# Performance work log

Hardware: AMD Instinct MI355X
Metric: run time of the kernel (lower is better)

## Reference

```python
import jax, jax.numpy as jnp
import numpy as np

B, S, H, D = 2, 2048, 16, 64
BS = 128          # block_size
NB = S // BS      # number of diagonal blocks
G = 128           # num_global_tokens
R = 64            # num_random_tokens
SCALE = 1.0 / float(D) ** 0.5


def setup_inputs() -> dict:
    key = jax.random.key(0)
    kq, kk, kv, kr = jax.random.split(key, 4)
    q = jax.random.normal(kq, (B, S, H, D), dtype=jnp.float32)
    k = jax.random.normal(kk, (B, S, H, D), dtype=jnp.float32)
    v = jax.random.normal(kv, (B, S, H, D), dtype=jnp.float32)
    attn_mask = jnp.zeros((B, H, S, S), dtype=jnp.float32)
    rand_indices = jax.random.randint(kr, (R,), 0, S, dtype=jnp.int32)
    return {"q": q, "k": k, "v": v, "attn_mask": attn_mask, "rand_indices": rand_indices}


def reference(q, k, v, attn_mask, rand_indices):
    # ---- diagonal block attention ----
    qb = q.reshape(B, NB, BS, H, D)
    kb = k.reshape(B, NB, BS, H, D)
    vb = v.reshape(B, NB, BS, H, D)
    scores = jnp.einsum('bnqhd,bnkhd->bnhqk', qb, kb) * SCALE  # (B,NB,H,BS,BS)
    mb = attn_mask.reshape(B, H, NB, BS, NB, BS)
    idx = jnp.arange(NB)
    diag = mb[:, :, idx, :, idx, :]                # (NB,B,H,BS,BS)
    scores = scores + jnp.transpose(diag, (1, 0, 2, 3, 4))
    w = jax.nn.softmax(scores, axis=-1)
    out = jnp.einsum('bnhqk,bnkhd->bnqhd', w, vb).reshape(B, S, H, D)

    # ---- global tokens attend to everything ----
    gq = q[:, :G]
    gv = v[:, :G]
    gs = jnp.einsum('bghd,bshd->bhgs', gq, k) * SCALE + attn_mask[:, :, :G, :]
    gw = jax.nn.softmax(gs, axis=-1)
    # faithful to torch einsum 'bhnm,bnhd->bnhd': v is indexed by the QUERY
    # axis, so this equals global_v * row-sum of softmax (== 1 numerically)
    out = out.at[:, :G].add(jnp.einsum('bhgs,bghd->bghd', gw, gv))

    # ---- random tokens attend to everything ----
    rq = q[:, rand_indices]                        # (B,R,H,D)
    rv = v[:, rand_indices]
    rs = jnp.einsum('brhd,bshd->bhrs', rq, k) * SCALE + attn_mask[:, :, rand_indices, :]
    rw = jax.nn.softmax(rs, axis=-1)
    # faithful to torch's size-1 broadcast in 'bhnm,bmhd->bnhd':
    # contribution = rand_v * row-sum of softmax
    rowsum = jnp.transpose(jnp.sum(rw, axis=-1), (0, 2, 1))  # (B,R,H)
    out = out.at[:, rand_indices].add(rv * rowsum[..., None])  # duplicate idx add, like the torch loop
    return out
```

## Files before the change

### kernel.cpp

```cpp
#include <hip/hip_runtime.h>
#include <stdint.h>

#define B_ 2
#define S_ 2048
#define H_ 16
#define D_ 64
#define BS_ 128
#define NB_ 16
#define R_ 64

typedef __bf16 bf16x8 __attribute__((ext_vector_type(8)));
typedef float f32x4 __attribute__((ext_vector_type(4)));

__device__ __forceinline__ uint16_t f2bf(float f) {
    uint32_t u = __builtin_bit_cast(uint32_t, f);
    u += 0x7fffu + ((u >> 16) & 1u);
    return (uint16_t)(u >> 16);
}

__global__ __launch_bounds__(256, 2) void bb_diag(
    const float* __restrict__ q, const float* __restrict__ k,
    const float* __restrict__ v, const float* __restrict__ mask,
    float* __restrict__ out)
{
    __shared__ __align__(16) uint8_t smem[49152];
    uint8_t* const k_lds  = smem;
    uint8_t* const p_lds  = smem;
    uint8_t* const vt_lds = smem + 32768;

    const int tid  = (int)threadIdx.x;
    const int w    = tid >> 6;
    const int lane = tid & 63;
    const int g    = lane >> 4;
    const int c    = lane & 15;

    const int blk = (int)blockIdx.x;
    const int h = blk & 15;
    const int n = (blk >> 4) & 15;
    const int b = blk >> 8;

    const int RS = H_ * D_;
    const size_t base = ((size_t)((b * S_ + n * BS_) * H_ + h)) * D_;
    const float* __restrict__ qg = q + base;
    const float* __restrict__ kg = k + base;
    const float* __restrict__ vg = v + base;
    float* __restrict__ og = out + base;

    #pragma unroll
    for (int it = 0; it < 8; ++it) {
        int i = it * 256 + tid;
        int row = i >> 4;
        int c4  = i & 15;
        f32x4 kv = *(const f32x4*)(kg + (size_t)row * RS + c4 * 4);
        uint32_t lo = (uint32_t)f2bf(kv[0]) | ((uint32_t)f2bf(kv[1]) << 16);
        uint32_t hi = (uint32_t)f2bf(kv[2]) | ((uint32_t)f2bf(kv[3]) << 16);
        uint32_t ka = ((uint32_t)(row * 128 + c4 * 8)) ^ ((row & 7) << 4);
        uint2 pk; pk.x = lo; pk.y = hi;
        *(uint2*)(k_lds + ka) = pk;

        f32x4 vv = *(const f32x4*)(vg + (size_t)row * RS + c4 * 4);
        #pragma unroll
        for (int jj = 0; jj < 4; ++jj) {
            int j = (jj + c4) & 3;
            int d = c4 * 4 + j;
            uint32_t va = ((uint32_t)(d * 256 + row * 2)) ^ ((d & 7) << 4);
            float vf = (j == 0) ? vv[0] : (j == 1) ? vv[1] : (j == 2) ? vv[2] : vv[3];
            *(uint16_t*)(vt_lds + va) = f2bf(vf);
        }
    }
    __syncthreads();

    bf16x8 qf[2][2];
    #pragma unroll
    for (int mt = 0; mt < 2; ++mt) {
        int row = (2 * w + mt) * 16 + c;
        const float* qrow = qg + (size_t)row * RS;
        #pragma unroll
        for (int ks = 0; ks < 2; ++ks) {
            const float* p0 = qrow + ks * 32 + g * 8;
            f32x4 x0 = *(const f32x4*)p0;
            f32x4 x1 = *(const f32x4*)(p0 + 4);
            union { bf16x8 v8; uint16_t us[8]; } cv;
            cv.us[0] = f2bf(x0[0]); cv.us[1] = f2bf(x0[1]);
            cv.us[2] = f2bf(x0[2]); cv.us[3] = f2bf(x0[3]);
            cv.us[4] = f2bf(x1[0]); cv.us[5] = f2bf(x1[1]);
            cv.us[6] = f2bf(x1[2]); cv.us[7] = f2bf(x1[3]);
            qf[mt][ks] = cv.v8;
        }
    }

    f32x4 acc[2][8];
    #pragma unroll
    for (int mt = 0; mt < 2; ++mt)
        #pragma unroll
        for (int nt = 0; nt < 8; ++nt)
            acc[mt][nt] = f32x4{0.f, 0.f, 0.f, 0.f};

    #pragma unroll
    for (int ks = 0; ks < 2; ++ks) {
        #pragma unroll
        for (int nt = 0; nt < 8; ++nt) {
            int krow = nt * 16 + c;
            uint32_t ka = ((uint32_t)(krow * 128 + ks * 64 + g * 16)) ^ ((krow & 7) << 4);
            bf16x8 bfr = *(const bf16x8*)(k_lds + ka);
            acc[0][nt] = __builtin_amdgcn_mfma_f32_16x16x32_bf16(qf[0][ks], bfr, acc[0][nt], 0, 0, 0);
            acc[1][nt] = __builtin_amdgcn_mfma_f32_16x16x32_bf16(qf[1][ks], bfr, acc[1][nt], 0, 0, 0);
        }
    }
    __syncthreads();

    const float* mb = mask + ((size_t)(b * H_ + h) * S_ + n * BS_) * S_ + (size_t)(n * BS_);
    float rcp_s[2][4];
    #pragma unroll
    for (int mt = 0; mt < 2; ++mt) {
        #pragma unroll
        for (int j = 0; j < 4; ++j) {
            int row = (2 * w + mt) * 16 + g * 4 + j;
            const float* mrow = mb + (size_t)row * S_;
            float s[8];
            float mx = -1e30f;
            #pragma unroll
            for (int nt = 0; nt < 8; ++nt) {
                s[nt] = acc[mt][nt][j] * 0.125f + mrow[nt * 16 + c];
                mx = fmaxf(mx, s[nt]);
            }
            #pragma unroll
            for (int t = 1; t < 16; t <<= 1) mx = fmaxf(mx, __shfl_xor(mx, t));
            float sum = 0.f;
            #pragma unroll
            for (int nt = 0; nt < 8; ++nt) {
                float p = __expf(s[nt] - mx);
                sum += p;
                uint32_t pa = ((uint32_t)(row * 256 + (nt * 16 + c) * 2)) ^ ((row & 7) << 4);
                *(uint16_t*)(p_lds + pa) = f2bf(p);
            }
            #pragma unroll
            for (int t = 1; t < 16; t <<= 1) sum += __shfl_xor(sum, t);
            rcp_s[mt][j] = 1.0f / sum;
        }
    }
    __syncthreads();

    f32x4 acc2[2][4];
    #pragma unroll
    for (int mt = 0; mt < 2; ++mt)
        #pragma unroll
        for (int nt = 0; nt < 4; ++nt)
            acc2[mt][nt] = f32x4{0.f, 0.f, 0.f, 0.f};

    #pragma unroll
    for (int kk = 0; kk < 4; ++kk) {
        bf16x8 af[2];
        #pragma unroll
        for (int mt = 0; mt < 2; ++mt) {
            int prow = (2 * w + mt) * 16 + c;
            uint32_t pa = ((uint32_t)(prow * 256 + kk * 64 + g * 16)) ^ ((prow & 7) << 4);
            af[mt] = *(const bf16x8*)(p_lds + pa);
        }
        #pragma unroll
        for (int nt = 0; nt < 4; ++nt) {
            int drow = nt * 16 + c;
            uint32_t va = ((uint32_t)(drow * 256 + kk * 64 + g * 16)) ^ ((drow & 7) << 4);
            bf16x8 bfr = *(const bf16x8*)(vt_lds + va);
            acc2[0][nt] = __builtin_amdgcn_mfma_f32_16x16x32_bf16(af[0], bfr, acc2[0][nt], 0, 0, 0);
            acc2[1][nt] = __builtin_amdgcn_mfma_f32_16x16x32_bf16(af[1], bfr, acc2[1][nt], 0, 0, 0);
        }
    }

    #pragma unroll
    for (int mt = 0; mt < 2; ++mt) {
        #pragma unroll
        for (int j = 0; j < 4; ++j) {
            int row = (2 * w + mt) * 16 + g * 4 + j;
            float rc = rcp_s[mt][j];
            #pragma unroll
            for (int nt = 0; nt < 4; ++nt) {
                int col = nt * 16 + c;
                float val = acc2[mt][nt][j] * rc;
                if (n == 0) val += vg[(size_t)row * RS + col];
                og[(size_t)row * RS + col] = val;
            }
        }
    }
}

__global__ __launch_bounds__(256) void bb_rand_add(
    const float* __restrict__ v, const int* __restrict__ ridx,
    float* __restrict__ out)
{
    int t = (int)(blockIdx.x * 256u + threadIdx.x);
    int d = t & 63;
    int h = (t >> 6) & 15;
    int r = (t >> 10) & 63;
    int b = t >> 16;
    int s = ridx[r];
    size_t off = ((size_t)((b * S_ + s) * H_ + h)) * D_ + d;
    atomicAdd(out + off, v[off]);
}

extern "C" void kernel_launch(void* const* d_in, const int* in_sizes, int n_in,
                              void* d_out, int out_size, void* d_ws, size_t ws_size,
                              hipStream_t stream) {
    const float* q    = (const float*)d_in[0];
    const float* k    = (const float*)d_in[1];
    const float* v    = (const float*)d_in[2];
    const float* mask = (const float*)d_in[3];
    const int*   ridx = (const int*)d_in[4];
    float* out = (float*)d_out;

    bb_diag<<<dim3(B_ * NB_ * H_), dim3(256), 0, stream>>>(q, k, v, mask, out);
    bb_rand_add<<<dim3((B_ * R_ * H_ * D_) / 256), dim3(256), 0, stream>>>(v, ridx, out);
}
```

Before: 617.8 us.

## Split query blocks in half and fold random-token add into attention kernel

Each workgroup now handles 64 query rows instead of 128, doubling the grid, cutting LDS use and raising the occupancy hint. The random-token contribution is counted per row in shared memory from ridx and applied as a coefficient on v in the epilogue, so the separate atomic-add kernel and its launch go away. The mask tile is prefetched into registers before the barrier, and bf16 conversion uses native casts instead of manual rounding. K and V staging is now done twice per diagonal block, once for each half.

```diff
diff --git a/kernel.cpp b/kernel.cpp
--- a/kernel.cpp
+++ b/kernel.cpp
@@ -10,23 +10,19 @@
 #define R_ 64
 
 typedef __bf16 bf16x8 __attribute__((ext_vector_type(8)));
-typedef float f32x4 __attribute__((ext_vector_type(4)));
+typedef __bf16 bf16x4 __attribute__((ext_vector_type(4)));
+typedef float  f32x4  __attribute__((ext_vector_type(4)));
 
-__device__ __forceinline__ uint16_t f2bf(float f) {
-    uint32_t u = __builtin_bit_cast(uint32_t, f);
-    u += 0x7fffu + ((u >> 16) & 1u);
-    return (uint16_t)(u >> 16);
-}
-
-__global__ __launch_bounds__(256, 2) void bb_diag(
+__global__ __launch_bounds__(256, 4) void bb_diag(
     const float* __restrict__ q, const float* __restrict__ k,
     const float* __restrict__ v, const float* __restrict__ mask,
-    float* __restrict__ out)
+    const int* __restrict__ ridx, float* __restrict__ out)
 {
-    __shared__ __align__(16) uint8_t smem[49152];
+    __shared__ __align__(16) uint8_t smem[33024];
     uint8_t* const k_lds  = smem;
     uint8_t* const p_lds  = smem;
-    uint8_t* const vt_lds = smem + 32768;
+    uint8_t* const vt_lds = smem + 16384;
+    int* const cnt = (int*)(smem + 32768);
 
     const int tid  = (int)threadIdx.x;
     const int w    = tid >> 6;
@@ -34,10 +30,12 @@
     const int g    = lane >> 4;
     const int c    = lane & 15;
 
-    const int blk = (int)blockIdx.x;
-    const int h = blk & 15;
-    const int n = (blk >> 4) & 15;
-    const int b = blk >> 8;
+    const int blk  = (int)blockIdx.x;
+    const int half = blk >> 9;
+    const int rest = blk & 511;
+    const int h = rest & 15;
+    const int n = (rest >> 4) & 15;
+    const int b = rest >> 8;
 
     const int RS = H_ * D_;
     const size_t base = ((size_t)((b * S_ + n * BS_) * H_ + h)) * D_;
@@ -46,17 +44,19 @@
     const float* __restrict__ vg = v + base;
     float* __restrict__ og = out + base;
 
+    if (tid < 64) cnt[tid] = 0;
+
     #pragma unroll
     for (int it = 0; it < 8; ++it) {
-        int i = it * 256 + tid;
+        int i   = it * 256 + tid;
         int row = i >> 4;
         int c4  = i & 15;
         f32x4 kv = *(const f32x4*)(kg + (size_t)row * RS + c4 * 4);
-        uint32_t lo = (uint32_t)f2bf(kv[0]) | ((uint32_t)f2bf(kv[1]) << 16);
-        uint32_t hi = (uint32_t)f2bf(kv[2]) | ((uint32_t)f2bf(kv[3]) << 16);
+        bf16x4 kb;
+        kb[0] = (__bf16)kv[0]; kb[1] = (__bf16)kv[1];
+        kb[2] = (__bf16)kv[2]; kb[3] = (__bf16)kv[3];
         uint32_t ka = ((uint32_t)(row * 128 + c4 * 8)) ^ ((row & 7) << 4);
-        uint2 pk; pk.x = lo; pk.y = hi;
-        *(uint2*)(k_lds + ka) = pk;
+        *(bf16x4*)(k_lds + ka) = kb;
 
         f32x4 vv = *(const f32x4*)(vg + (size_t)row * RS + c4 * 4);
         #pragma unroll
@@ -65,37 +65,47 @@
             int d = c4 * 4 + j;
             uint32_t va = ((uint32_t)(d * 256 + row * 2)) ^ ((d & 7) << 4);
             float vf = (j == 0) ? vv[0] : (j == 1) ? vv[1] : (j == 2) ? vv[2] : vv[3];
-            *(uint16_t*)(vt_lds + va) = f2bf(vf);
+            *(__bf16*)(vt_lds + va) = (__bf16)vf;
+        }
+    }
+
+    bf16x8 qf[2];
+    {
+        int row_l = w * 16 + c;
+        const float* qrow = qg + (size_t)(half * 64 + row_l) * RS;
+        #pragma unroll
+        for (int ks = 0; ks < 2; ++ks) {
+            f32x4 x0 = *(const f32x4*)(qrow + ks * 32 + g * 8);
+            f32x4 x1 = *(const f32x4*)(qrow + ks * 32 + g * 8 + 4);
+            union { bf16x8 v8; __bf16 e[8]; } cv;
+            #pragma unroll
+            for (int j = 0; j < 4; ++j) { cv.e[j] = (__bf16)x0[j]; cv.e[4 + j] = (__bf16)x1[j]; }
+            qf[ks] = cv.v8;
+        }
+    }
+
+    float m[4][8];
+    {
+        const float* mb = mask + ((size_t)(b * H_ + h) * S_ + n * BS_ + half * 64 + w * 16) * S_
+                               + (size_t)(n * BS_);
+        #pragma unroll
+        for (int j = 0; j < 4; ++j) {
+            const float* mrow = mb + (size_t)(g * 4 + j) * S_;
+            #pragma unroll
+            for (int nt = 0; nt < 8; ++nt) m[j][nt] = mrow[nt * 16 + c];
         }
     }
     __syncthreads();
 
-    bf16x8 qf[2][2];
-    #pragma unroll
-    for (int mt = 0; mt < 2; ++mt) {
-        int row = (2 * w + mt) * 16 + c;
-        const float* qrow = qg + (size_t)row * RS;
-        #pragma unroll
-        for (int ks = 0; ks < 2; ++ks) {
-            const float* p0 = qrow + ks * 32 + g * 8;
-            f32x4 x0 = *(const f32x4*)p0;
-            f32x4 x1 = *(const f32x4*)(p0 + 4);
-            union { bf16x8 v8; uint16_t us[8]; } cv;
-            cv.us[0] = f2bf(x0[0]); cv.us[1] = f2bf(x0[1]);
-            cv.us[2] = f2bf(x0[2]); cv.us[3] = f2bf(x0[3]);
-            cv.us[4] = f2bf(x1[0]); cv.us[5] = f2bf(x1[1]);
-            cv.us[6] = f2bf(x1[2]); cv.us[7] = f2bf(x1[3]);
-            qf[mt][ks] = cv.v8;
-        }
+    if (tid < 64) {
+        int s = ridx[tid];
+        int lo = n * BS_ + half * 64;
+        if (s >= lo && s < lo + 64) atomicAdd(&cnt[s - lo], 1);
     }
 
-    f32x4 acc[2][8];
+    f32x4 acc[8];
     #pragma unroll
-    for (int mt = 0; mt < 2; ++mt)
-        #pragma unroll
-        for (int nt = 0; nt < 8; ++nt)
-            acc[mt][nt] = f32x4{0.f, 0.f, 0.f, 0.f};
-
+    for (int nt = 0; nt < 8; ++nt) acc[nt] = f32x4{0.f, 0.f, 0.f, 0.f};
     #pragma unroll
     for (int ks = 0; ks < 2; ++ks) {
         #pragma unroll
@@ -103,99 +113,69 @@
             int krow = nt * 16 + c;
             uint32_t ka = ((uint32_t)(krow * 128 + ks * 64 + g * 16)) ^ ((krow & 7) << 4);
             bf16x8 bfr = *(const bf16x8*)(k_lds + ka);
-            acc[0][nt] = __builtin_amdgcn_mfma_f32_16x16x32_bf16(qf[0][ks], bfr, acc[0][nt], 0, 0, 0);
-            acc[1][nt] = __builtin_amdgcn_mfma_f32_16x16x32_bf16(qf[1][ks], bfr, acc[1][nt], 0, 0, 0);
+            acc[nt] = __builtin_amdgcn_mfma_f32_16x16x32_bf16(qf[ks], bfr, acc[nt], 0, 0, 0);
         }
     }
     __syncthreads();
 
-    const float* mb = mask + ((size_t)(b * H_ + h) * S_ + n * BS_) * S_ + (size_t)(n * BS_);
-    float rcp_s[2][4];
+    float rcp_s[4];
     #pragma unroll
-    for (int mt = 0; mt < 2; ++mt) {
+    for (int j = 0; j < 4; ++j) {
+        int row = w * 16 + g * 4 + j;
+        float s[8];
+        float mx = -1e30f;
         #pragma unroll
-        for (int j = 0; j < 4; ++j) {
-            int row = (2 * w + mt) * 16 + g * 4 + j;
-            const float* mrow = mb + (size_t)row * S_;
-            float s[8];
-            float mx = -1e30f;
-            #pragma unroll
-            for (int nt = 0; nt < 8; ++nt) {
-                s[nt] = acc[mt][nt][j] * 0.125f + mrow[nt * 16 + c];
-                mx = fmaxf(mx, s[nt]);
-            }
-            #pragma unroll
-            for (int t = 1; t < 16; t <<= 1) mx = fmaxf(mx, __shfl_xor(mx, t));
-            float sum = 0.f;
-            #pragma unroll
-            for (int nt = 0; nt < 8; ++nt) {
-                float p = __expf(s[nt] - mx);
-                sum += p;
-                uint32_t pa = ((uint32_t)(row * 256 + (nt * 16 + c) * 2)) ^ ((row & 7) << 4);
-                *(uint16_t*)(p_lds + pa) = f2bf(p);
-            }
-            #pragma unroll
-            for (int t = 1; t < 16; t <<= 1) sum += __shfl_xor(sum, t);
-            rcp_s[mt][j] = 1.0f / sum;
+        for (int nt = 0; nt < 8; ++nt) {
+            s[nt] = acc[nt][j] * 0.125f + m[j][nt];
+            mx = fmaxf(mx, s[nt]);
         }
+        #pragma unroll
+        for (int t = 1; t < 16; t <<= 1) mx = fmaxf(mx, __shfl_xor(mx, t));
+        float sum = 0.f;
+        #pragma unroll
+        for (int nt = 0; nt < 8; ++nt) {
+            float p = __expf(s[nt] - mx);
+            sum += p;
+            uint32_t pa = ((uint32_t)(row * 256 + (nt * 16 + c) * 2)) ^ ((row & 7) << 4);
+            *(__bf16*)(p_lds + pa) = (__bf16)p;
+        }
+        #pragma unroll
+        for (int t = 1; t < 16; t <<= 1) sum += __shfl_xor(sum, t);
+        rcp_s[j] = 1.0f / sum;
     }
     __syncthreads();
 
-    f32x4 acc2[2][4];
+    f32x4 acc2[4];
     #pragma unroll
-    for (int mt = 0; mt < 2; ++mt)
-        #pragma unroll
-        for (int nt = 0; nt < 4; ++nt)
-            acc2[mt][nt] = f32x4{0.f, 0.f, 0.f, 0.f};
-
+    for (int nt = 0; nt < 4; ++nt) acc2[nt] = f32x4{0.f, 0.f, 0.f, 0.f};
     #pragma unroll
     for (int kk = 0; kk < 4; ++kk) {
-        bf16x8 af[2];
-        #pragma unroll
-        for (int mt = 0; mt < 2; ++mt) {
-            int prow = (2 * w + mt) * 16 + c;
-            uint32_t pa = ((uint32_t)(prow * 256 + kk * 64 + g * 16)) ^ ((prow & 7) << 4);
-            af[mt] = *(const bf16x8*)(p_lds + pa);
-        }
+        int prow = w * 16 + c;
+        uint32_t pa = ((uint32_t)(prow * 256 + kk * 64 + g * 16)) ^ ((prow & 7) << 4);
+        bf16x8 af = *(const bf16x8*)(p_lds + pa);
         #pragma unroll
         for (int nt = 0; nt < 4; ++nt) {
             int drow = nt * 16 + c;
             uint32_t va = ((uint32_t)(drow * 256 + kk * 64 + g * 16)) ^ ((drow & 7) << 4);
             bf16x8 bfr = *(const bf16x8*)(vt_lds + va);
-            acc2[0][nt] = __builtin_amdgcn_mfma_f32_16x16x32_bf16(af[0], bfr, acc2[0][nt], 0, 0, 0);
-            acc2[1][nt] = __builtin_amdgcn_mfma_f32_16x16x32_bf16(af[1], bfr, acc2[1][nt], 0, 0, 0);
+            acc2[nt] = __builtin_amdgcn_mfma_f32_16x16x32_bf16(af, bfr, acc2[nt], 0, 0, 0);
         }
     }
 
     #pragma unroll
-    for (int mt = 0; mt < 2; ++mt) {
+    for (int j = 0; j < 4; ++j) {
+        int r_l = w * 16 + g * 4 + j;
+        int r_t = half * 64 + r_l;
+        float rc = rcp_s[j];
+        float coef = (float)(cnt[r_l] + ((n == 0) ? 1 : 0));
         #pragma unroll
-        for (int j = 0; j < 4; ++j) {
-            int row = (2 * w + mt) * 16 + g * 4 + j;
-            float rc = rcp_s[mt][j];
-            #pragma unroll
-            for (int nt = 0; nt < 4; ++nt) {
-                int col = nt * 16 + c;
-                float val = acc2[mt][nt][j] * rc;
-                if (n == 0) val += vg[(size_t)row * RS + col];
-                og[(size_t)row * RS + col] = val;
-            }
+        for (int nt = 0; nt < 4; ++nt) {
+            int col = nt * 16 + c;
+            float val = acc2[nt][j] * rc;
+            if (coef != 0.f) val += coef * vg[(size_t)r_t * RS + col];
+            og[(size_t)r_t * RS + col] = val;
         }
     }
-}
-
-__global__ __launch_bounds__(256) void bb_rand_add(
-    const float* __restrict__ v, const int* __restrict__ ridx,
-    float* __restrict__ out)
-{
-    int t = (int)(blockIdx.x * 256u + threadIdx.x);
-    int d = t & 63;
-    int h = (t >> 6) & 15;
-    int r = (t >> 10) & 63;
-    int b = t >> 16;
-    int s = ridx[r];
-    size_t off = ((size_t)((b * S_ + s) * H_ + h)) * D_ + d;
-    atomicAdd(out + off, v[off]);
 }
 
 extern "C" void kernel_launch(void* const* d_in, const int* in_sizes, int n_in,
@@ -208,6 +188,5 @@
     const int*   ridx = (const int*)d_in[4];
     float* out = (float*)d_out;
 
-    bb_diag<<<dim3(B_ * NB_ * H_), dim3(256), 0, stream>>>(q, k, v, mask, out);
-    bb_rand_add<<<dim3((B_ * R_ * H_ * D_) / 256), dim3(256), 0, stream>>>(v, ridx, out);
+    bb_diag<<<dim3(B_ * NB_ * H_ * 2), dim3(256), 0, stream>>>(q, k, v, mask, ridx, out);
 }
```

Result: no change. 613.2 us (-0.7%).
